# Optimization experiments

Hardware: AMD Instinct MI355X
Metric: run time of the kernel (lower is better)

Reference implementation:

```python
import jax, jax.numpy as jnp
import numpy as np

B, S, E, H = 8, 1024, 1024, 16
EPS = 1e-3  # tf.keras LayerNormalization default epsilon


def setup_inputs() -> dict:
    key = jax.random.key(0)
    ks = jax.random.split(key, 5)
    x = jax.random.normal(ks[0], (B, S, E), dtype=jnp.float32)
    Wq = jax.random.normal(ks[1], (E, E), dtype=jnp.float32) * 0.02
    Wk = jax.random.normal(ks[2], (E, E), dtype=jnp.float32) * 0.02
    Wv = jax.random.normal(ks[3], (E, E), dtype=jnp.float32) * 0.02
    # original init is zeros; use small random values so the bias path is exercised
    rel_table = jax.random.normal(ks[4], (2 * S - 1, H), dtype=jnp.float32) * 0.02
    gamma = jnp.ones((E,), dtype=jnp.float32)
    beta = jnp.zeros((E,), dtype=jnp.float32)
    return {"x": x, "Wq": Wq, "Wk": Wk, "Wv": Wv, "rel_table": rel_table,
            "gamma": gamma, "beta": beta}


def reference(x, Wq, Wk, Wv, rel_table, gamma, beta):
    b, s, e = x.shape
    h = rel_table.shape[1]
    scale = e ** (-0.5)  # NOTE: scales by full emb_size, not head_dim (faithful)

    def split_heads(t):  # (b, s, e) -> (b, h, s, d)
        return t.reshape(b, s, h, -1).transpose(0, 2, 1, 3)

    q = split_heads(x @ Wq)
    k = split_heads(x @ Wk)
    v = split_heads(x @ Wv)

    attn = jnp.einsum("bhqd,bhkd->bhqk", q, k) * scale
    attn = jax.nn.softmax(attn, axis=-1)

    # relative bias: gather then the exact (quirky) reshape sequence of the original
    r = jnp.arange(s)
    rel_index = jnp.clip(r[None, :] - r[:, None] + (s - 1), 0, 2 * s - 2)  # (s, s)
    bias = rel_table[rel_index]              # (s, s, h)
    bias = bias.reshape(-1).reshape(h, s, s)  # faithful flat-order reinterpretation
    attn = attn + bias[None]  # added POST-softmax, as in the original

    out = jnp.einsum("bhqk,bhkd->bhqd", attn, v)
    out = out.transpose(0, 2, 1, 3).reshape(b, s, e)

    # LayerNorm over last axis
    mu = jnp.mean(out, axis=-1, keepdims=True)
    var = jnp.var(out, axis=-1, keepdims=True)
    out = (out - mu) / jnp.sqrt(var + EPS) * gamma + beta
    return out
```

## Files before the change

kernel.cpp:

```cpp
#include <hip/hip_runtime.h>
#include <hip/hip_bf16.h>

#define PB 8
#define PS 1024
#define PE 1024
#define PH 16
#define PD 64
#define EPSLN 1e-3f
#define QSCALE 0.04508422f

typedef __attribute__((ext_vector_type(8))) short bf16x8;
typedef __attribute__((ext_vector_type(4))) float f32x4;
typedef __attribute__((ext_vector_type(16))) float f32x16;

__device__ __forceinline__ unsigned short f2bf(float f) {
    unsigned int u = __float_as_uint(f);
    u += 0x7FFFu + ((u >> 16) & 1u);
    return (unsigned short)(u >> 16);
}

__device__ __forceinline__ void gload_lds16(const void* g, void* l) {
    __builtin_amdgcn_global_load_lds(
        (const __attribute__((address_space(1))) unsigned int*)g,
        (__attribute__((address_space(3))) unsigned int*)l,
        16, 0, 0);
}

__device__ __forceinline__ unsigned int cvtpk_bf16(float lo, float hi) {
    unsigned int r;
    asm("v_cvt_pk_bf16_f32 %0, %1, %2" : "=v"(r) : "v"(lo), "v"(hi));
    return r;
}

__device__ __forceinline__ void plswap(unsigned int& a, unsigned int& b) {
    asm("v_permlane32_swap_b32 %0, %1" : "+v"(a), "+v"(b));
}

__device__ __forceinline__ float exp2_raw(float x) {
    float r;
    asm("v_exp_f32 %0, %1" : "=v"(r) : "v"(x));
    return r;
}

#define SWZF(row, chunk) (((chunk) ^ ((row) & 7) ^ (((row) >> 3) & 3)))

__global__ __launch_bounds__(256) void conv_x(
    const float* __restrict__ X, unsigned short* __restrict__ Xb)
{
    const size_t i = (size_t)blockIdx.x * 256 + threadIdx.x;
    const float4* p = reinterpret_cast<const float4*>(X) + i * 2;
    float4 a = p[0], b = p[1];
    unsigned short r[8];
    r[0] = f2bf(a.x); r[1] = f2bf(a.y); r[2] = f2bf(a.z); r[3] = f2bf(a.w);
    r[4] = f2bf(b.x); r[5] = f2bf(b.y); r[6] = f2bf(b.z); r[7] = f2bf(b.w);
    *reinterpret_cast<uint4*>(Xb + i * 8) = *reinterpret_cast<const uint4*>(r);
}

__global__ __launch_bounds__(256) void conv_w(
    const float* __restrict__ Wq, const float* __restrict__ Wk,
    const float* __restrict__ Wv, unsigned short* __restrict__ Wtb)
{
    const int proj = blockIdx.z;
    const float* W = (proj == 0) ? Wq : (proj == 1) ? Wk : Wv;
    const float sc = (proj == 0) ? QSCALE : 1.0f;
    __shared__ float tile[32][33];
    const int n0 = blockIdx.x * 32, k0 = blockIdx.y * 32;
    const int tx = threadIdx.x & 31, ty = threadIdx.x >> 5;
#pragma unroll
    for (int i = 0; i < 4; ++i)
        tile[ty + i * 8][tx] = W[(size_t)(k0 + ty + i * 8) * PE + n0 + tx];
    __syncthreads();
#pragma unroll
    for (int i = 0; i < 4; ++i)
        Wtb[(size_t)(proj * 1024 + n0 + ty + i * 8) * 1024 + k0 + tx] =
            f2bf(tile[tx][ty + i * 8] * sc);
}

__global__ __launch_bounds__(256) void conv_rel(
    const float* __restrict__ rel, unsigned short* __restrict__ relbf)
{
    const int i = blockIdx.x * 1024 + threadIdx.x * 4;
#pragma unroll
    for (int k = 0; k < 4; ++k)
        if (i + k < (2 * PS - 1) * PH) relbf[i + k] = f2bf(rel[i + k]);
}

__global__ __launch_bounds__(256) void qkv_mfma(
    const unsigned short* __restrict__ Xb,
    const unsigned short* __restrict__ Wtb,
    unsigned short* __restrict__ QKV)
{
    const int orig = blockIdx.x;
    const int wg = (orig & 7) * 192 + (orig >> 3);
    const int nblk = wg % 24, mblk = wg / 24;
    const int m0 = mblk * 128, n0 = nblk * 128;

    __shared__ __align__(16) unsigned short As[128 * 64];
    __shared__ __align__(16) unsigned short Bs[128 * 64];

    const int t = threadIdx.x;
    const int w = t >> 6, l = t & 63;
    const int lane15 = l & 15, lhi = l >> 4;
    const int wm = w >> 1, wn = w & 1;

    f32x4 acc[4][4] = {};

    for (int k0 = 0; k0 < 1024; k0 += 64) {
        __syncthreads();
#pragma unroll
        for (int c = 0; c < 4; ++c) {
            const int ci = (w * 4 + c) * 64 + l;
            const int r = ci >> 3;
            const int srccl = (ci & 7) ^ (r & 7);
            gload_lds16(Xb  + (size_t)(m0 + r) * 1024 + k0 + srccl * 8, &As[ci * 8]);
            gload_lds16(Wtb + (size_t)(n0 + r) * 1024 + k0 + srccl * 8, &Bs[ci * 8]);
        }
        __syncthreads();
#pragma unroll
        for (int kk = 0; kk < 2; ++kk) {
            bf16x8 af[4], bf[4];
#pragma unroll
            for (int mi = 0; mi < 4; ++mi) {
                const int row = wm * 64 + mi * 16 + lane15;
                af[mi] = *reinterpret_cast<const bf16x8*>(
                    &As[row * 64 + (((kk * 4 + lhi) ^ (row & 7)) << 3)]);
            }
#pragma unroll
            for (int ni = 0; ni < 4; ++ni) {
                const int row = wn * 64 + ni * 16 + lane15;
                bf[ni] = *reinterpret_cast<const bf16x8*>(
                    &Bs[row * 64 + (((kk * 4 + lhi) ^ (row & 7)) << 3)]);
            }
#pragma unroll
            for (int mi = 0; mi < 4; ++mi)
#pragma unroll
                for (int ni = 0; ni < 4; ++ni)
                    acc[mi][ni] = __builtin_amdgcn_mfma_f32_16x16x32_bf16(
                        af[mi], bf[ni], acc[mi][ni], 0, 0, 0);
        }
    }
#pragma unroll
    for (int mi = 0; mi < 4; ++mi)
#pragma unroll
        for (int ni = 0; ni < 4; ++ni)
#pragma unroll
            for (int r = 0; r < 4; ++r) {
                const int gr = m0 + wm * 64 + mi * 16 + lhi * 4 + r;
                const int gc = n0 + wn * 64 + ni * 16 + lane15;
                QKV[(size_t)gr * 3072 + gc] = f2bf(acc[mi][ni][r]);
            }
}

__global__ __launch_bounds__(256) void vtrans(
    const unsigned short* __restrict__ QKV, unsigned short* __restrict__ VT)
{
    const int j0 = blockIdx.x * 64, b = blockIdx.y, h = blockIdx.z;
    __shared__ unsigned short tile[64][72];
    const int t = threadIdx.x;

#pragma unroll
    for (int it = 0; it < 2; ++it) {
        const int jr = it * 32 + (t >> 3), dc = t & 7;
        uint4 d = *reinterpret_cast<const uint4*>(
            QKV + ((size_t)(b * PS + j0 + jr)) * 3072 + 2048 + h * 64 + dc * 8);
        *reinterpret_cast<uint4*>(&tile[jr][dc * 8]) = d;
    }
    __syncthreads();
    const int d = t & 63, jc = t >> 6;
    unsigned short out[16];
#pragma unroll
    for (int k = 0; k < 16; ++k) out[k] = tile[jc * 16 + k][d];
    unsigned short* dst = VT + ((size_t)((h * 8 + b) * 64 + d)) * 1024 + j0 + jc * 16;
    *reinterpret_cast<uint4*>(dst)     = *reinterpret_cast<const uint4*>(out);
    *reinterpret_cast<uint4*>(dst + 8) = *reinterpret_cast<const uint4*>(out + 8);
}

__global__ __launch_bounds__(256) void attn_mfma(
    const unsigned short* __restrict__ qkv,
    const unsigned short* __restrict__ VT,
    const unsigned short* __restrict__ relbf,
    float* __restrict__ O)
{
    __shared__ __align__(16) unsigned short Ks[2][64 * 64];
    __shared__ __align__(16) unsigned short Vt[2][64 * 64];

    const int orig = blockIdx.x;
    const int wg = (orig & 7) * 128 + (orig >> 3);
    const int qt = wg & 7;
    const int h  = (wg >> 3) & 15;
    const int b  = wg >> 7;

    const int t = threadIdx.x;
    const int w = t >> 6, l = t & 63;
    const int lane31 = l & 31, hi = l >> 5;

    const int qrow_g = qt * 128 + w * 32 + lane31;

    bf16x8 qf[4];
    {
        const unsigned short* qp =
            qkv + ((size_t)(b * PS) + qrow_g) * 3072 + h * 64 + hi * 8;
#pragma unroll
        for (int dw = 0; dw < 4; ++dw)
            qf[dw] = *reinterpret_cast<const bf16x8*>(qp + dw * 16);
    }

    const unsigned short* Kg = qkv + (size_t)(b * PS) * 3072 + 1024 + h * 64;
    const unsigned short* Vg = VT + ((size_t)((h * 8 + b) * 64)) * 1024;

    const int s1 = (h << 6) | (qrow_g >> 4);
    const int s2hi = (qrow_g & 15) << 6;
    const unsigned short* relp = relbf + (size_t)(s2hi - s1 + PS - 1) * PH + hi * 8;

    f32x16 accP[2] = {};
    f32x16 accB[2] = {};
    f32x16 accL = {};
    bf16x8 ones;
#pragma unroll
    for (int i = 0; i < 8; ++i) ones[i] = (short)0x3F80;

#define ATTN_STAGE(buf, j0)                                                          \
    {                                                                                \
        _Pragma("unroll")                                                            \
        for (int it = 0; it < 2; ++it) {                                             \
            const int ci = it * 256 + t;                                             \
            const int r = ci >> 3;                                                   \
            const int scl = SWZF(r, ci & 7);                                         \
            gload_lds16(Kg + (size_t)((j0) + r) * 3072 + scl * 8, &Ks[buf][ci * 8]); \
            gload_lds16(Vg + (size_t)r * 1024 + (j0) + scl * 8, &Vt[buf][ci * 8]);   \
        }                                                                            \
    }

#define SM_FINISH(sc, pfA, pfB)                                                      \
    {                                                                                \
        float p[16];                                                                 \
        _Pragma("unroll")                                                            \
        for (int r = 0; r < 16; ++r) p[r] = exp2_raw((sc)[r]);                       \
        unsigned int a0 = cvtpk_bf16(p[0],  p[1]),  a1 = cvtpk_bf16(p[2],  p[3]);    \
        unsigned int b0 = cvtpk_bf16(p[4],  p[5]),  b1 = cvtpk_bf16(p[6],  p[7]);    \
        unsigned int c0 = cvtpk_bf16(p[8],  p[9]),  c1 = cvtpk_bf16(p[10], p[11]);   \
        unsigned int d0 = cvtpk_bf16(p[12], p[13]), d1 = cvtpk_bf16(p[14], p[15]);   \
        plswap(a0, b0); plswap(a1, b1);                                              \
        plswap(c0, d0); plswap(c1, d1);                                              \
        union { unsigned int u[4]; bf16x8 v; } pk0, pk1;                             \
        pk0.u[0] = a0; pk0.u[1] = a1; pk0.u[2] = b0; pk0.u[3] = b1;                  \
        pk1.u[0] = c0; pk1.u[1] = c1; pk1.u[2] = d0; pk1.u[3] = d1;                  \
        (pfA) = pk0.v; (pfB) = pk1.v;                                                \
    }

#define PV_STEP(jw, pf)                                                              \
    {                                                                                \
        accL = __builtin_amdgcn_mfma_f32_32x32x16_bf16((pf), ones, accL, 0, 0, 0);   \
        _Pragma("unroll")                                                            \
        for (int dt = 0; dt < 2; ++dt) {                                             \
            const int row = dt * 32 + lane31;                                        \
            bf16x8 bV = *reinterpret_cast<const bf16x8*>(                            \
                &Vt[cur][row * 64 + (SWZF(row, (jw) * 2 + hi) << 3)]);               \
            accP[dt] = __builtin_amdgcn_mfma_f32_32x32x16_bf16(                      \
                (pf), bV, accP[dt], 0, 0, 0);                                        \
            accB[dt] = __builtin_amdgcn_mfma_f32_32x32x16_bf16(                      \
                af[jw], bV, accB[dt], 0, 0, 0);                                      \
        }                                                                            \
    }

    ATTN_STAGE(0, 0)

    for (int tt = 0; tt < 16; ++tt) {
        const int cur = tt & 1;
        const int j0 = tt * 64;

        bf16x8 af[4];
        __builtin_amdgcn_sched_barrier(0);
#pragma unroll
        for (int jw = 0; jw < 4; ++jw)
            af[jw] = *reinterpret_cast<const bf16x8*>(relp + j0 + jw * 16);
        __builtin_amdgcn_sched_barrier(0);
        if (tt < 15) {
            ATTN_STAGE(cur ^ 1, j0 + 64)
            __builtin_amdgcn_sched_barrier(0);
            asm volatile("s_waitcnt vmcnt(8)" ::: "memory");
        } else {
            asm volatile("s_waitcnt vmcnt(4)" ::: "memory");
        }
        __builtin_amdgcn_sched_barrier(0);
        __builtin_amdgcn_s_barrier();
        __builtin_amdgcn_sched_barrier(0);

        f32x16 sc0 = {}, sc1 = {};
        __builtin_amdgcn_s_setprio(1);
#pragma unroll
        for (int dw = 0; dw < 4; ++dw) {
            const int row = lane31;
            bf16x8 aK = *reinterpret_cast<const bf16x8*>(
                &Ks[cur][row * 64 + (SWZF(row, dw * 2 + hi) << 3)]);
            sc0 = __builtin_amdgcn_mfma_f32_32x32x16_bf16(aK, qf[dw], sc0, 0, 0, 0);
        }
#pragma unroll
        for (int dw = 0; dw < 4; ++dw) {
            const int row = 32 + lane31;
            bf16x8 aK = *reinterpret_cast<const bf16x8*>(
                &Ks[cur][row * 64 + (SWZF(row, dw * 2 + hi) << 3)]);
            sc1 = __builtin_amdgcn_mfma_f32_32x32x16_bf16(aK, qf[dw], sc1, 0, 0, 0);
        }
        __builtin_amdgcn_s_setprio(0);

        bf16x8 pf0, pf1, pf2, pf3;
        SM_FINISH(sc0, pf0, pf1)

        __builtin_amdgcn_s_setprio(1);
        PV_STEP(0, pf0)
        PV_STEP(1, pf1)
        __builtin_amdgcn_s_setprio(0);

        SM_FINISH(sc1, pf2, pf3)

        __builtin_amdgcn_s_setprio(1);
        PV_STEP(2, pf2)
        PV_STEP(3, pf3)
        __builtin_amdgcn_s_setprio(0);

        __builtin_amdgcn_s_barrier();
    }
#undef ATTN_STAGE
#undef SM_FINISH
#undef PV_STEP

#pragma unroll
    for (int dt = 0; dt < 2; ++dt)
#pragma unroll
        for (int r = 0; r < 16; ++r) {
            const int rl = (r & 3) + 8 * (r >> 2) + 4 * hi;
            O[((size_t)(b * PS + qt * 128 + w * 32 + rl)) * PE + h * 64 + dt * 32 + lane31]
                = accP[dt][r] / accL[r] + accB[dt][r];
        }
}

__global__ __launch_bounds__(256) void layernorm_inplace(
    float* __restrict__ O,
    const float* __restrict__ gamma,
    const float* __restrict__ beta)
{
    const int row = blockIdx.x;
    float* p = O + (size_t)row * PE;
    const int t = threadIdx.x;

    float4 x = reinterpret_cast<float4*>(p)[t];
    float s  = x.x + x.y + x.z + x.w;
    float s2 = x.x * x.x + x.y * x.y + x.z * x.z + x.w * x.w;

#pragma unroll
    for (int off = 1; off < 64; off <<= 1) {
        s  += __shfl_xor(s, off, 64);
        s2 += __shfl_xor(s2, off, 64);
    }
    __shared__ float red[2][4];
    const int wid = t >> 6;
    if ((t & 63) == 0) { red[0][wid] = s; red[1][wid] = s2; }
    __syncthreads();
    const float ts  = red[0][0] + red[0][1] + red[0][2] + red[0][3];
    const float ts2 = red[1][0] + red[1][1] + red[1][2] + red[1][3];

    const float mu  = ts * (1.f / PE);
    const float var = ts2 * (1.f / PE) - mu * mu;
    const float inv = rsqrtf(var + EPSLN);

    const float4 g  = reinterpret_cast<const float4*>(gamma)[t];
    const float4 bb = reinterpret_cast<const float4*>(beta)[t];
    float4 y;
    y.x = (x.x - mu) * inv * g.x + bb.x;
    y.y = (x.y - mu) * inv * g.y + bb.y;
    y.z = (x.z - mu) * inv * g.z + bb.z;
    y.w = (x.w - mu) * inv * g.w + bb.w;
    reinterpret_cast<float4*>(p)[t] = y;
}

extern "C" void kernel_launch(void* const* d_in, const int* in_sizes, int n_in,
                              void* d_out, int out_size, void* d_ws, size_t ws_size,
                              hipStream_t stream) {
    (void)in_sizes; (void)n_in; (void)out_size; (void)ws_size;
    const float* x     = (const float*)d_in[0];
    const float* Wq    = (const float*)d_in[1];
    const float* Wk    = (const float*)d_in[2];
    const float* Wv    = (const float*)d_in[3];
    const float* rel   = (const float*)d_in[4];
    const float* gamma = (const float*)d_in[5];
    const float* beta  = (const float*)d_in[6];
    float* out = (float*)d_out;

    char* ws = (char*)d_ws;
    unsigned short* Xb    = (unsigned short*)ws;
    unsigned short* Wtb   = (unsigned short*)(ws + 16777216);
    unsigned short* QKV   = (unsigned short*)(ws + 23068672);
    unsigned short* VT    = (unsigned short*)(ws + 73400320);
    unsigned short* relbf = (unsigned short*)ws;

    conv_x<<<4096, 256, 0, stream>>>(x, Xb);
    conv_w<<<dim3(32, 32, 3), 256, 0, stream>>>(Wq, Wk, Wv, Wtb);
    qkv_mfma<<<1536, 256, 0, stream>>>(Xb, Wtb, QKV);
    conv_rel<<<32, 256, 0, stream>>>(rel, relbf);
    vtrans<<<dim3(16, 8, 16), 256, 0, stream>>>(QKV, VT);
    attn_mfma<<<1024, 256, 0, stream>>>(QKV, VT, relbf, out);
    layernorm_inplace<<<PB * PS, 256, 0, stream>>>(out, gamma, beta);
}
```

Baseline: 169.2 us.

## Double-buffer QKV GEMM with 256x128 tiles and split-phase MFMA scheduling

Rewrites the QKV projection GEMM to use 512-thread blocks with 256x128 output tiles, double-buffered LDS stages loaded via global_load_lds, and a two-phase schedule per k-step. Loads for step k+2 are issued between the two MFMA halves, with explicit waitcnt, barriers and setprio. The aim is to hide global-to-LDS latency and raise operand reuse per block. In exchange it uses much more LDS (96 KB per block), limiting occupancy, and relies on fragile hand-tuned wait counts.

```diff
diff --git a/kernel.cpp b/kernel.cpp
--- a/kernel.cpp
+++ b/kernel.cpp
@@ -85,68 +85,138 @@
         if (i + k < (2 * PS - 1) * PH) relbf[i + k] = f2bf(rel[i + k]);
 }
 
-__global__ __launch_bounds__(256) void qkv_mfma(
+__global__ __launch_bounds__(512, 2) void qkv_mfma(
     const unsigned short* __restrict__ Xb,
     const unsigned short* __restrict__ Wtb,
     unsigned short* __restrict__ QKV)
 {
     const int orig = blockIdx.x;
-    const int wg = (orig & 7) * 192 + (orig >> 3);
+    const int wg = (orig & 7) * 96 + (orig >> 3);
     const int nblk = wg % 24, mblk = wg / 24;
-    const int m0 = mblk * 128, n0 = nblk * 128;
-
-    __shared__ __align__(16) unsigned short As[128 * 64];
-    __shared__ __align__(16) unsigned short Bs[128 * 64];
+    const int m0 = mblk * 256, n0 = nblk * 128;
+
+    __shared__ __align__(16) unsigned short As[2][256 * 64];
+    __shared__ __align__(16) unsigned short Bs[2][128 * 64];
 
     const int t = threadIdx.x;
-    const int w = t >> 6, l = t & 63;
+    const int l = t & 63, w = t >> 6;
     const int lane15 = l & 15, lhi = l >> 4;
-    const int wm = w >> 1, wn = w & 1;
-
-    f32x4 acc[4][4] = {};
-
-    for (int k0 = 0; k0 < 1024; k0 += 64) {
-        __syncthreads();
-#pragma unroll
-        for (int c = 0; c < 4; ++c) {
-            const int ci = (w * 4 + c) * 64 + l;
-            const int r = ci >> 3;
-            const int srccl = (ci & 7) ^ (r & 7);
-            gload_lds16(Xb  + (size_t)(m0 + r) * 1024 + k0 + srccl * 8, &As[ci * 8]);
-            gload_lds16(Wtb + (size_t)(n0 + r) * 1024 + k0 + srccl * 8, &Bs[ci * 8]);
-        }
-        __syncthreads();
-#pragma unroll
-        for (int kk = 0; kk < 2; ++kk) {
-            bf16x8 af[4], bf[4];
-#pragma unroll
-            for (int mi = 0; mi < 4; ++mi) {
-                const int row = wm * 64 + mi * 16 + lane15;
-                af[mi] = *reinterpret_cast<const bf16x8*>(
-                    &As[row * 64 + (((kk * 4 + lhi) ^ (row & 7)) << 3)]);
+    const int wm = w >> 2, wn = w & 3;
+
+    f32x4 acc[8][2] = {};
+
+#define QSTAGE_AH(kt, c, h)                                                     \
+    {                                                                           \
+        _Pragma("unroll")                                                       \
+        for (int rr = 0; rr < 2; ++rr) {                                        \
+            const int ci = (h) * 1024 + rr * 512 + t;                           \
+            const int r = ci >> 3;                                              \
+            const int scl = (ci & 7) ^ (r & 7);                                 \
+            gload_lds16(Xb + (size_t)(m0 + r) * 1024 + (kt) * 64 + scl * 8,     \
+                        &As[c][ci * 8]);                                        \
+        }                                                                       \
+    }
+#define QSTAGE_B(kt, c)                                                         \
+    {                                                                           \
+        _Pragma("unroll")                                                       \
+        for (int rr = 0; rr < 2; ++rr) {                                        \
+            const int ci = rr * 512 + t;                                        \
+            const int r = ci >> 3;                                              \
+            const int scl = (ci & 7) ^ (r & 7);                                 \
+            gload_lds16(Wtb + (size_t)(n0 + r) * 1024 + (kt) * 64 + scl * 8,    \
+                        &Bs[c][ci * 8]);                                        \
+        }                                                                       \
+    }
+
+    QSTAGE_B(0, 0) QSTAGE_AH(0, 0, 0) QSTAGE_AH(0, 0, 1)
+    QSTAGE_B(1, 1) QSTAGE_AH(1, 1, 0) QSTAGE_AH(1, 1, 1)
+    asm volatile("s_waitcnt vmcnt(6)" ::: "memory");
+    __builtin_amdgcn_sched_barrier(0);
+    __builtin_amdgcn_s_barrier();
+
+    for (int kt = 0; kt < 16; ++kt) {
+        const int c = kt & 1;
+        bf16x8 afr[8][2], bfr[2][2];
+
+#pragma unroll
+        for (int mi = 0; mi < 4; ++mi)
+#pragma unroll
+            for (int kk = 0; kk < 2; ++kk) {
+                const int row = wm * 128 + mi * 16 + lane15;
+                afr[mi][kk] = *reinterpret_cast<const bf16x8*>(
+                    &As[c][row * 64 + (((kk * 4 + lhi) ^ (row & 7)) << 3)]);
             }
 #pragma unroll
-            for (int ni = 0; ni < 4; ++ni) {
-                const int row = wn * 64 + ni * 16 + lane15;
-                bf[ni] = *reinterpret_cast<const bf16x8*>(
-                    &Bs[row * 64 + (((kk * 4 + lhi) ^ (row & 7)) << 3)]);
+        for (int ni = 0; ni < 2; ++ni)
+#pragma unroll
+            for (int kk = 0; kk < 2; ++kk) {
+                const int row = wn * 32 + ni * 16 + lane15;
+                bfr[ni][kk] = *reinterpret_cast<const bf16x8*>(
+                    &Bs[c][row * 64 + (((kk * 4 + lhi) ^ (row & 7)) << 3)]);
             }
-#pragma unroll
-            for (int mi = 0; mi < 4; ++mi)
-#pragma unroll
-                for (int ni = 0; ni < 4; ++ni)
+        asm volatile("s_waitcnt lgkmcnt(8)" ::: "memory");
+        __builtin_amdgcn_s_barrier();
+        asm volatile("s_waitcnt lgkmcnt(0)" ::: "memory");
+        __builtin_amdgcn_sched_barrier(0);
+        __builtin_amdgcn_s_setprio(1);
+#pragma unroll
+        for (int mi = 0; mi < 4; ++mi)
+#pragma unroll
+            for (int ni = 0; ni < 2; ++ni)
+#pragma unroll
+                for (int kk = 0; kk < 2; ++kk)
                     acc[mi][ni] = __builtin_amdgcn_mfma_f32_16x16x32_bf16(
-                        af[mi], bf[ni], acc[mi][ni], 0, 0, 0);
-        }
-    }
-#pragma unroll
-    for (int mi = 0; mi < 4; ++mi)
-#pragma unroll
-        for (int ni = 0; ni < 4; ++ni)
+                        afr[mi][kk], bfr[ni][kk], acc[mi][ni], 0, 0, 0);
+        __builtin_amdgcn_s_setprio(0);
+        __builtin_amdgcn_sched_barrier(0);
+        __builtin_amdgcn_s_barrier();
+
+#pragma unroll
+        for (int mi = 4; mi < 8; ++mi)
+#pragma unroll
+            for (int kk = 0; kk < 2; ++kk) {
+                const int row = wm * 128 + mi * 16 + lane15;
+                afr[mi][kk] = *reinterpret_cast<const bf16x8*>(
+                    &As[c][row * 64 + (((kk * 4 + lhi) ^ (row & 7)) << 3)]);
+            }
+        if (kt < 14) {
+            QSTAGE_B(kt + 2, c)
+            QSTAGE_AH(kt + 2, c, 0)
+            QSTAGE_AH(kt + 2, c, 1)
+        }
+        __builtin_amdgcn_s_barrier();
+        asm volatile("s_waitcnt lgkmcnt(0)" ::: "memory");
+        __builtin_amdgcn_sched_barrier(0);
+        __builtin_amdgcn_s_setprio(1);
+#pragma unroll
+        for (int mi = 4; mi < 8; ++mi)
+#pragma unroll
+            for (int ni = 0; ni < 2; ++ni)
+#pragma unroll
+                for (int kk = 0; kk < 2; ++kk)
+                    acc[mi][ni] = __builtin_amdgcn_mfma_f32_16x16x32_bf16(
+                        afr[mi][kk], bfr[ni][kk], acc[mi][ni], 0, 0, 0);
+        __builtin_amdgcn_s_setprio(0);
+        __builtin_amdgcn_sched_barrier(0);
+        if (kt < 14) {
+            asm volatile("s_waitcnt vmcnt(6)" ::: "memory");
+        } else if (kt == 14) {
+            asm volatile("s_waitcnt vmcnt(0)" ::: "memory");
+        }
+        __builtin_amdgcn_sched_barrier(0);
+        __builtin_amdgcn_s_barrier();
+    }
+#undef QSTAGE_AH
+#undef QSTAGE_B
+
+#pragma unroll
+    for (int mi = 0; mi < 8; ++mi)
+#pragma unroll
+        for (int ni = 0; ni < 2; ++ni)
 #pragma unroll
             for (int r = 0; r < 4; ++r) {
-                const int gr = m0 + wm * 64 + mi * 16 + lhi * 4 + r;
-                const int gc = n0 + wn * 64 + ni * 16 + lane15;
+                const int gr = m0 + wm * 128 + mi * 16 + lhi * 4 + r;
+                const int gc = n0 + wn * 32 + ni * 16 + lane15;
                 QKV[(size_t)gr * 3072 + gc] = f2bf(acc[mi][ni][r]);
             }
 }
@@ -396,7 +466,7 @@
 
     conv_x<<<4096, 256, 0, stream>>>(x, Xb);
     conv_w<<<dim3(32, 32, 3), 256, 0, stream>>>(Wq, Wk, Wv, Wtb);
-    qkv_mfma<<<1536, 256, 0, stream>>>(Xb, Wtb, QKV);
+    qkv_mfma<<<768, 512, 0, stream>>>(Xb, Wtb, QKV);
     conv_rel<<<32, 256, 0, stream>>>(rel, relbf);
     vtrans<<<dim3(16, 8, 16), 256, 0, stream>>>(QKV, VT);
     attn_mfma<<<1024, 256, 0, stream>>>(QKV, VT, relbf, out);
```

After: 174.2 us. 2.9% more time.
